# Kernel optimization log

Hardware: AMD Instinct MI355X
Metric: run time of the kernel (lower is better)

Reference implementation:

```python
import jax, jax.numpy as jnp
import numpy as np
import math

NSEG = 4
SAMPLE_RATE = 16  # curve samples per bezier segment
SHARPNESS = 150.0


def _control_radians():
    n = NSEG
    theta = math.pi * 2 / (4 * n) + math.atan(math.tan(2 * math.pi / (4 * n)) / 3)
    r = []
    for i in range(n):
        r += [2 * math.pi / n * i, 2 * math.pi / n * i + theta, 2 * math.pi / n * (i + 1) - theta]
    return jnp.asarray(np.asarray(r, dtype=np.float32).reshape(n, 3))


def sdf_extruded_bezier(quaternion, translation, points, control_polygon, bez_weights, height):
    # quaternion [B,K,4], translation [B,K,3], points [B,M,3],
    # control_polygon [B,K,nseg,3,2], bez_weights [B,K,nseg,2], height [B,K]
    B, K, _ = quaternion.shape
    p = points[:, :, None, :] - translation[:, None, :, :]            # [B,M,K,3]
    q = quaternion[:, None, :, :]
    qn = q / jnp.sqrt(jnp.sum(q * q, -1, keepdims=True) + 1e-8)
    w, qv = qn[..., :1], -qn[..., 1:]                                  # conjugate -> world->local
    t2 = 2.0 * jnp.cross(qv, p)
    pl = p + w * t2 + jnp.cross(qv, t2)                                # local coords [B,M,K,3]
    p2d, pz = pl[..., :2], pl[..., 2]
    # rational cubic bezier per segment: P0,P1,P2 from this segment, P3 = next segment's P0
    P0 = control_polygon[:, :, :, 0, :]
    P1 = control_polygon[:, :, :, 1, :]
    P2 = control_polygon[:, :, :, 2, :]
    P3 = jnp.roll(P0, -1, axis=2)
    ts = jnp.linspace(0.0, 1.0, SAMPLE_RATE, endpoint=False)           # [S]
    b0 = (1 - ts) ** 3
    b1 = 3 * (1 - ts) ** 2 * ts
    b2 = 3 * (1 - ts) * ts ** 2
    b3 = ts ** 3
    w1 = bez_weights[..., 0:1]                                          # [B,K,nseg,1]
    w2 = bez_weights[..., 1:2]
    den = b0 + w1 * b1 + w2 * b2 + b3                                   # [B,K,nseg,S]
    num = (P0[..., None, :] * b0[:, None]
           + P1[..., None, :] * (w1[..., None] * b1[:, None])
           + P2[..., None, :] * (w2[..., None] * b2[:, None])
           + P3[..., None, :] * b3[:, None])                            # [B,K,nseg,S,2]
    curve = (num / den[..., None]).reshape(B, K, NSEG * SAMPLE_RATE, 2)
    rel = curve[:, None] - p2d[..., None, :]                            # [B,M,K,S*nseg,2]
    d2 = jnp.sum(rel * rel, -1)
    dmin = jnp.sqrt(jnp.min(d2, -1) + 1e-12)                            # unsigned 2D distance
    nxt = jnp.roll(rel, -1, axis=-2)
    cross = rel[..., 0] * nxt[..., 1] - rel[..., 1] * nxt[..., 0]
    dot = jnp.sum(rel * nxt, -1)
    winding = jnp.sum(jnp.arctan2(cross, dot), -1) / (2 * math.pi)
    sdf2d = jnp.where(jnp.abs(winding) > 0.5, -dmin, dmin)
    dz = jnp.abs(pz) - jnp.abs(height)[:, None, :]
    sdf = (jnp.minimum(jnp.maximum(sdf2d, dz), 0.0)
           + jnp.sqrt(jnp.maximum(sdf2d, 0.0) ** 2 + jnp.maximum(dz, 0.0) ** 2 + 1e-12))
    return sdf, dmin


def setup_inputs() -> dict:
    key = jax.random.key(0)
    k1, k2, k3, k4 = jax.random.split(key, 4)
    B, M, K, C = 4, 2048, 64, 64
    P = 4 + 3 + 1 + NSEG * 3 + NSEG * 2  # 28
    return {
        "sample_point_coordinates": jax.random.uniform(k1, (B, M, 3), jnp.float32, -1.0, 1.0),
        "primitive_parameters": 0.3 * jax.random.normal(k2, (B, P, K), jnp.float32),
        "intersection_layer_weights": jax.random.uniform(k3, (B, K, C), jnp.float32),
        "union_layer_weights": jax.random.uniform(k4, (B, C), jnp.float32),
        "is_training": 1,
    }


def reference(sample_point_coordinates, primitive_parameters, intersection_layer_weights, union_layer_weights, is_training):
    pp = jnp.swapaxes(primitive_parameters, 1, 2)                       # [B,K,P]
    B, K, _ = pp.shape
    quaternion = pp[..., :4]
    translation = pp[..., 4:7]
    height = pp[..., 7]
    radius = jnp.abs(pp[..., 8:8 + NSEG * 3]).reshape(B, K, NSEG, 3)
    rad = _control_radians()[None, None]                                # [1,1,nseg,3]
    control_polygon = jnp.stack([jnp.cos(rad) * radius, jnp.sin(rad) * radius], -1)
    bez_weights = jnp.abs(pp[..., 8 + NSEG * 3:]).reshape(B, K, NSEG, 2)
    primitive_sdf, support_distances = sdf_extruded_bezier(
        quaternion, translation, sample_point_coordinates, control_polygon, bez_weights, height)
    primitive_occ = jax.nn.sigmoid(-primitive_sdf * SHARPNESS)          # [B,M,K]
    # occupancy_pre_intersection = w*occ + (1-w)*1 = 1 - w*(1-occ), fused
    w_int = intersection_layer_weights[:, None]                         # [B,1,K,C]
    pre_i = 1.0 - w_int * (1.0 - primitive_occ[..., None])              # [B,M,K,C]
    if is_training:
        sw = jax.lax.stop_gradient(jax.nn.softmax(pre_i * -40.0, axis=-2))
        inter = jnp.sum(sw * pre_i, -2)                                 # soft-min -> [B,M,C]
    else:
        inter = jnp.min(pre_i, -2)
    pre_u = union_layer_weights[:, None, :] * inter
    if is_training:
        sw2 = jax.lax.stop_gradient(jax.nn.softmax(pre_u * 40.0, axis=-1))
        occupancies = jnp.sum(sw2 * pre_u, -1)                          # soft-max -> [B,M]
    else:
        occupancies = jnp.max(pre_u, -1)
    return occupancies, primitive_sdf, inter, support_distances
```

## Files before the change

### kernel.cpp

```cpp
#include <hip/hip_runtime.h>
#include <math.h>


#define NB 4
#define NM 2048
#define NK 64
#define NC 64
#define NS 64
#define PPB 4

#define OCC_OFF   0
#define SDF_OFF   8192
#define INTER_OFF 532480
#define SUP_OFF   1056768

#define CT 0.86285621096f
#define ST 0.50544946275f

#define L2E_40  57.70780163555852f
#define L2E_150 216.40425613334447f

__global__ __launch_bounds__(256) void curve_table_kernel(
    const float* __restrict__ pp,
    float2* __restrict__ wcurve)
{
    const int b    = blockIdx.x;
    const int lane = threadIdx.x & 63;
    const int seg  = threadIdx.x >> 6;
    const int nseg = (seg + 1) & 3;
    const float* __restrict__ ppb = pp + b * (28 * NK);
    const int k = lane;

    const float r0 = fabsf(ppb[(8 + seg * 3 + 0) * NK + k]);
    const float r1 = fabsf(ppb[(8 + seg * 3 + 1) * NK + k]);
    const float r2 = fabsf(ppb[(8 + seg * 3 + 2) * NK + k]);
    const float rn = fabsf(ppb[(8 + nseg * 3 + 0) * NK + k]);
    const float w1 = fabsf(ppb[(20 + seg * 2 + 0) * NK + k]);
    const float w2 = fabsf(ppb[(20 + seg * 2 + 1) * NK + k]);

    const float c0x[4] = { 1.f, 0.f, -1.f,  0.f };
    const float c0y[4] = { 0.f, 1.f,  0.f, -1.f };
    const float c1x[4] = {  CT, -ST, -CT,  ST };
    const float c1y[4] = {  ST,  CT, -ST, -CT };
    const float c2x[4] = {  ST, -CT, -ST,  CT };
    const float c2y[4] = {  CT,  ST, -CT, -ST };

    const float P0x = c0x[seg] * r0,  P0y = c0y[seg] * r0;
    const float P1x = c1x[seg] * r1,  P1y = c1y[seg] * r1;
    const float P2x = c2x[seg] * r2,  P2y = c2y[seg] * r2;
    const float P3x = c0x[nseg] * rn, P3y = c0y[nseg] * rn;

    #pragma unroll
    for (int j = 0; j < 16; ++j) {
        const float t  = (float)j * 0.0625f;
        const float u  = 1.f - t;
        const float b0 = u * u * u;
        const float b1 = 3.f * u * u * t;
        const float b2 = 3.f * u * t * t;
        const float b3 = t * t * t;
        const float wb1 = w1 * b1, wb2 = w2 * b2;
        const float inv = __builtin_amdgcn_rcpf(b0 + wb1 + wb2 + b3);
        const int s = seg * 16 + j;
        wcurve[(b * NS + s) * NK + k] = make_float2(
            (P0x * b0 + P1x * wb1 + P2x * wb2 + P3x * b3) * inv,
            (P0y * b0 + P1y * wb1 + P2y * wb2 + P3y * b3) * inv);
    }
}

__global__ __launch_bounds__(256) void extrude_net_kernel(
    const float* __restrict__ pts,
    const float* __restrict__ pp,
    const float* __restrict__ Wint,
    const float* __restrict__ Uw,
    const float2* __restrict__ wcurve,
    float* __restrict__ out)
{
    __shared__ __align__(16) float2 s_curve[NS][NK];
    __shared__ float s_om[PPB][NK];

    const int tid  = threadIdx.x;
    const int lane = tid & 63;
    const int wv   = tid >> 6;
    const int gpt  = blockIdx.x * PPB + wv;
    const int b    = gpt >> 11;
    const float* __restrict__ ppb = pp + b * (28 * NK);

    {
        const float4* __restrict__ src = (const float4*)wcurve + b * (NS * NK / 2);
        float4* dst = (float4*)&s_curve[0][0];
        #pragma unroll
        for (int i = 0; i < 8; ++i)
            dst[i * 256 + tid] = src[i * 256 + tid];
    }
    __syncthreads();

    const float ptx = pts[gpt * 3 + 0];
    const float pty = pts[gpt * 3 + 1];
    const float ptz = pts[gpt * 3 + 2];
    {
        const int k = lane;
        const float q0 = ppb[0 * NK + k], q1 = ppb[1 * NK + k];
        const float q2 = ppb[2 * NK + k], q3 = ppb[3 * NK + k];
        const float trx = ppb[4 * NK + k], try_ = ppb[5 * NK + k], trz = ppb[6 * NK + k];
        const float h   = ppb[7 * NK + k];

        const float px = ptx - trx, py = pty - try_, pz = ptz - trz;
        const float inv = __builtin_amdgcn_rsqf(q0 * q0 + q1 * q1 + q2 * q2 + q3 * q3 + 1e-8f);
        const float w  = q0 * inv;
        const float vx = -q1 * inv, vy = -q2 * inv, vz = -q3 * inv;
        const float t2x = 2.f * (vy * pz - vz * py);
        const float t2y = 2.f * (vz * px - vx * pz);
        const float t2z = 2.f * (vx * py - vy * px);
        const float plx = px + w * t2x + (vy * t2z - vz * t2y);
        const float ply = py + w * t2y + (vz * t2x - vx * t2z);
        const float plz = pz + w * t2z + (vx * t2y - vy * t2x);

        const float2* __restrict__ col = &s_curve[0][k];

        const float2 cfirst = col[0];
        float rx = cfirst.x - plx;
        float ry = cfirst.y - ply;
        const float r0x = rx, r0y = ry;
        bool apos = ry > 0.f;
        const bool pos0 = apos;
        int   wn  = 0;
        float d2a = rx * rx + ry * ry;
        float d2b = 3.4e38f;
        #pragma unroll
        for (int s = 1; s < NS; ++s) {
            const float2 cn = col[s * NK];
            const float nx = cn.x - plx;
            const float ny = cn.y - ply;
            const float cr = rx * ny - ry * nx;
            const bool bpos = ny > 0.f;
            const bool cpos = cr > 0.f;
            const bool cneg = cr < 0.f;
            wn += ((!apos) & bpos & cpos) ? 1 : 0;
            wn -= (apos & (!bpos) & cneg) ? 1 : 0;
            const float d2 = nx * nx + ny * ny;
            if (s & 1) d2b = fminf(d2b, d2); else d2a = fminf(d2a, d2);
            apos = bpos; rx = nx; ry = ny;
        }
        {
            const float cr = rx * r0y - ry * r0x;
            wn += ((!apos) & pos0 & (cr > 0.f)) ? 1 : 0;
            wn -= (apos & (!pos0) & (cr < 0.f)) ? 1 : 0;
        }
        const float dmin  = sqrtf(fminf(d2a, d2b) + 1e-12f);
        const float sdf2d = (wn != 0) ? -dmin : dmin;
        const float dz    = fabsf(plz) - fabsf(h);
        const float mx    = fmaxf(sdf2d, dz);
        const float e1    = fmaxf(sdf2d, 0.f);
        const float e2    = fmaxf(dz, 0.f);
        const float sdf   = fminf(mx, 0.f) + sqrtf(e1 * e1 + e2 * e2 + 1e-12f);

        out[SDF_OFF + gpt * NK + k] = sdf;
        out[SUP_OFF + gpt * NK + k] = dmin;
        s_om[wv][k] = __builtin_amdgcn_rcpf(1.f + exp2f(-sdf * L2E_150));
    }
    __syncthreads();

    {
        const float4* __restrict__ wsrc = (const float4*)(Wint + b * (NK * NC));
        float4* wdst = (float4*)&s_curve[0][0];
        #pragma unroll
        for (int i = 0; i < 4; ++i)
            wdst[i * 256 + tid] = wsrc[i * 256 + tid];
    }
    __syncthreads();

    {
        const int c = lane;
        const float* __restrict__ WbL = (const float*)&s_curve[0][0];
        const float* __restrict__ omw = s_om[wv];
        float srun = 0.f, trun = 0.f;
        #pragma unroll
        for (int kk = 0; kk < NK; ++kk) {
            const float om  = omw[kk];
            const float pre = fmaf(-WbL[kk * NC + c], om, 1.f);
            const float e   = exp2f(pre * -L2E_40);
            srun += e;
            trun = fmaf(e, pre, trun);
        }
        const float inter = trun * __builtin_amdgcn_rcpf(srun);
        out[INTER_OFF + gpt * NC + c] = inter;

        const float pu = Uw[b * NC + c] * inter;
        float umax = pu;
        #pragma unroll
        for (int off = 32; off > 0; off >>= 1)
            umax = fmaxf(umax, __shfl_xor(umax, off, 64));
        const float e = exp2f((pu - umax) * L2E_40);
        float s1 = e, s2 = e * pu;
        #pragma unroll
        for (int off = 32; off > 0; off >>= 1) {
            s1 += __shfl_xor(s1, off, 64);
            s2 += __shfl_xor(s2, off, 64);
        }
        if (lane == 0) out[OCC_OFF + gpt] = s2 * __builtin_amdgcn_rcpf(s1);
    }
}

extern "C" void kernel_launch(void* const* d_in, const int* in_sizes, int n_in,
                              void* d_out, int out_size, void* d_ws, size_t ws_size,
                              hipStream_t stream) {
    const float* pts  = (const float*)d_in[0];
    const float* pp   = (const float*)d_in[1];
    const float* Wint = (const float*)d_in[2];
    const float* Uw   = (const float*)d_in[3];
    float*  out    = (float*)d_out;
    float2* wcurve = (float2*)d_ws;

    curve_table_kernel<<<NB, 256, 0, stream>>>(pp, wcurve);
    const int grid = (NB * NM) / PPB;
    extrude_net_kernel<<<grid, 256, 0, stream>>>(pts, pp, Wint, Uw, wcurve, out);
}
```

Measured before the change: 88.86 us.

## Fuse curve table computation into main kernel and preload Wint into separate LDS

Removes the separate curve-table kernel, so each block computes the rational Bezier samples directly into shared memory. The intersection weights are loaded into their own shared buffer at the start, which removes a later reload and one barrier. This eliminates one launch and the global workspace round trip. In exchange, every block recomputes the curve table and uses more shared memory per block, which may lower occupancy.

New measurement: 92.23 us. 1.04x slower.

```diff
diff --git a/kernel.cpp b/kernel.cpp
--- a/kernel.cpp
+++ b/kernel.cpp
@@ -20,62 +20,15 @@
 #define L2E_40  57.70780163555852f
 #define L2E_150 216.40425613334447f
 
-__global__ __launch_bounds__(256) void curve_table_kernel(
-    const float* __restrict__ pp,
-    float2* __restrict__ wcurve)
-{
-    const int b    = blockIdx.x;
-    const int lane = threadIdx.x & 63;
-    const int seg  = threadIdx.x >> 6;
-    const int nseg = (seg + 1) & 3;
-    const float* __restrict__ ppb = pp + b * (28 * NK);
-    const int k = lane;
-
-    const float r0 = fabsf(ppb[(8 + seg * 3 + 0) * NK + k]);
-    const float r1 = fabsf(ppb[(8 + seg * 3 + 1) * NK + k]);
-    const float r2 = fabsf(ppb[(8 + seg * 3 + 2) * NK + k]);
-    const float rn = fabsf(ppb[(8 + nseg * 3 + 0) * NK + k]);
-    const float w1 = fabsf(ppb[(20 + seg * 2 + 0) * NK + k]);
-    const float w2 = fabsf(ppb[(20 + seg * 2 + 1) * NK + k]);
-
-    const float c0x[4] = { 1.f, 0.f, -1.f,  0.f };
-    const float c0y[4] = { 0.f, 1.f,  0.f, -1.f };
-    const float c1x[4] = {  CT, -ST, -CT,  ST };
-    const float c1y[4] = {  ST,  CT, -ST, -CT };
-    const float c2x[4] = {  ST, -CT, -ST,  CT };
-    const float c2y[4] = {  CT,  ST, -CT, -ST };
-
-    const float P0x = c0x[seg] * r0,  P0y = c0y[seg] * r0;
-    const float P1x = c1x[seg] * r1,  P1y = c1y[seg] * r1;
-    const float P2x = c2x[seg] * r2,  P2y = c2y[seg] * r2;
-    const float P3x = c0x[nseg] * rn, P3y = c0y[nseg] * rn;
-
-    #pragma unroll
-    for (int j = 0; j < 16; ++j) {
-        const float t  = (float)j * 0.0625f;
-        const float u  = 1.f - t;
-        const float b0 = u * u * u;
-        const float b1 = 3.f * u * u * t;
-        const float b2 = 3.f * u * t * t;
-        const float b3 = t * t * t;
-        const float wb1 = w1 * b1, wb2 = w2 * b2;
-        const float inv = __builtin_amdgcn_rcpf(b0 + wb1 + wb2 + b3);
-        const int s = seg * 16 + j;
-        wcurve[(b * NS + s) * NK + k] = make_float2(
-            (P0x * b0 + P1x * wb1 + P2x * wb2 + P3x * b3) * inv,
-            (P0y * b0 + P1y * wb1 + P2y * wb2 + P3y * b3) * inv);
-    }
-}
-
 __global__ __launch_bounds__(256) void extrude_net_kernel(
     const float* __restrict__ pts,
     const float* __restrict__ pp,
     const float* __restrict__ Wint,
     const float* __restrict__ Uw,
-    const float2* __restrict__ wcurve,
     float* __restrict__ out)
 {
     __shared__ __align__(16) float2 s_curve[NS][NK];
+    __shared__ __align__(16) float  s_wb[NK * NC];
     __shared__ float s_om[PPB][NK];
 
     const int tid  = threadIdx.x;
@@ -86,11 +39,51 @@
     const float* __restrict__ ppb = pp + b * (28 * NK);
 
     {
-        const float4* __restrict__ src = (const float4*)wcurve + b * (NS * NK / 2);
-        float4* dst = (float4*)&s_curve[0][0];
+        const float4* __restrict__ wsrc = (const float4*)(Wint + b * (NK * NC));
+        float4* wdst = (float4*)&s_wb[0];
         #pragma unroll
-        for (int i = 0; i < 8; ++i)
-            dst[i * 256 + tid] = src[i * 256 + tid];
+        for (int i = 0; i < 4; ++i)
+            wdst[i * 256 + tid] = wsrc[i * 256 + tid];
+    }
+
+    {
+        const int k    = lane;
+        const int seg  = wv;
+        const int nseg = (seg + 1) & 3;
+        const float r0 = fabsf(ppb[(8 + seg * 3 + 0) * NK + k]);
+        const float r1 = fabsf(ppb[(8 + seg * 3 + 1) * NK + k]);
+        const float r2 = fabsf(ppb[(8 + seg * 3 + 2) * NK + k]);
+        const float rn = fabsf(ppb[(8 + nseg * 3 + 0) * NK + k]);
+        const float w1 = fabsf(ppb[(20 + seg * 2 + 0) * NK + k]);
+        const float w2 = fabsf(ppb[(20 + seg * 2 + 1) * NK + k]);
+
+        const float c0x[4] = { 1.f, 0.f, -1.f,  0.f };
+        const float c0y[4] = { 0.f, 1.f,  0.f, -1.f };
+        const float c1x[4] = {  CT, -ST, -CT,  ST };
+        const float c1y[4] = {  ST,  CT, -ST, -CT };
+        const float c2x[4] = {  ST, -CT, -ST,  CT };
+        const float c2y[4] = {  CT,  ST, -CT, -ST };
+
+        const float P0x = c0x[seg] * r0,  P0y = c0y[seg] * r0;
+        const float P1x = c1x[seg] * r1,  P1y = c1y[seg] * r1;
+        const float P2x = c2x[seg] * r2,  P2y = c2y[seg] * r2;
+        const float P3x = c0x[nseg] * rn, P3y = c0y[nseg] * rn;
+
+        #pragma unroll
+        for (int j = 0; j < 16; ++j) {
+            const float t  = (float)j * 0.0625f;
+            const float u  = 1.f - t;
+            const float b0 = u * u * u;
+            const float b1 = 3.f * u * u * t;
+            const float b2 = 3.f * u * t * t;
+            const float b3 = t * t * t;
+            const float wb1 = w1 * b1, wb2 = w2 * b2;
+            const float inv = __builtin_amdgcn_rcpf(b0 + wb1 + wb2 + b3);
+            const int s = seg * 16 + j;
+            s_curve[s][k] = make_float2(
+                (P0x * b0 + P1x * wb1 + P2x * wb2 + P3x * b3) * inv,
+                (P0y * b0 + P1y * wb1 + P2y * wb2 + P3y * b3) * inv);
+        }
     }
     __syncthreads();
 
@@ -133,10 +126,8 @@
             const float ny = cn.y - ply;
             const float cr = rx * ny - ry * nx;
             const bool bpos = ny > 0.f;
-            const bool cpos = cr > 0.f;
-            const bool cneg = cr < 0.f;
-            wn += ((!apos) & bpos & cpos) ? 1 : 0;
-            wn -= (apos & (!bpos) & cneg) ? 1 : 0;
+            wn += ((!apos) & bpos & (cr > 0.f)) ? 1 : 0;
+            wn -= (apos & (!bpos) & (cr < 0.f)) ? 1 : 0;
             const float d2 = nx * nx + ny * ny;
             if (s & 1) d2b = fminf(d2b, d2); else d2a = fminf(d2a, d2);
             apos = bpos; rx = nx; ry = ny;
@@ -161,17 +152,8 @@
     __syncthreads();
 
     {
-        const float4* __restrict__ wsrc = (const float4*)(Wint + b * (NK * NC));
-        float4* wdst = (float4*)&s_curve[0][0];
-        #pragma unroll
-        for (int i = 0; i < 4; ++i)
-            wdst[i * 256 + tid] = wsrc[i * 256 + tid];
-    }
-    __syncthreads();
-
-    {
         const int c = lane;
-        const float* __restrict__ WbL = (const float*)&s_curve[0][0];
+        const float* __restrict__ WbL = s_wb;
         const float* __restrict__ omw = s_om[wv];
         float srun = 0.f, trun = 0.f;
         #pragma unroll
@@ -208,10 +190,8 @@
     const float* pp   = (const float*)d_in[1];
     const float* Wint = (const float*)d_in[2];
     const float* Uw   = (const float*)d_in[3];
-    float*  out    = (float*)d_out;
-    float2* wcurve = (float2*)d_ws;
+    float* out = (float*)d_out;
 
-    curve_table_kernel<<<NB, 256, 0, stream>>>(pp, wcurve);
     const int grid = (NB * NM) / PPB;
-    extrude_net_kernel<<<grid, 256, 0, stream>>>(pts, pp, Wint, Uw, wcurve, out);
+    extrude_net_kernel<<<grid, 256, 0, stream>>>(pts, pp, Wint, Uw, out);
 }
```
